# Kernel optimization log

Hardware: AMD Instinct MI355X
Metric: run time of the kernel (lower is better)

## Reference

```python
import jax, jax.numpy as jnp
import numpy as np

VOCAB, HID, L, HEADS, INTER, MAXSEQ, NCLS = 30522, 128, 2, 2, 512, 512, 2
HEAD = HID // HEADS
B, S = 128, 512


def _tlin(x, W, b):
    # TernaryLinear: threshold-quantize W to {-1,0,1} with per-tensor scale,
    # then ordinary linear. delta = 0.7*mean|W|, alpha = mean|W| over kept entries.
    absW = jnp.abs(W)
    delta = 0.7 * jnp.mean(absW)
    mask = (absW > delta).astype(W.dtype)
    alpha = jnp.sum(absW * mask) / jnp.maximum(jnp.sum(mask), 1.0)
    Wq = jnp.sign(W) * mask * alpha  # [out, in]
    return jnp.einsum('...i,oi->...o', x, Wq) + b


def _ln(x, g, b, eps=1e-5):
    m = jnp.mean(x, axis=-1, keepdims=True)
    v = jnp.var(x, axis=-1, keepdims=True)
    return (x - m) * jax.lax.rsqrt(v + eps) * g + b


def setup_inputs() -> dict:
    key = jax.random.key(0)
    ks = iter(jax.random.split(key, 64))
    n = lambda shape, s=0.02: jax.random.normal(next(ks), shape, dtype=jnp.float32) * s
    inp = {
        'input_ids': jax.random.randint(next(ks), (B, S), 0, VOCAB, dtype=jnp.int32).astype(jnp.int64),
        'tok_emb': n((VOCAB, HID)),
        'pos_emb': n((MAXSEQ, HID)),
        'ln_g': jnp.ones((HID,), jnp.float32), 'ln_b': jnp.zeros((HID,), jnp.float32),
        'qw': n((L, HID, HID)), 'qb': jnp.zeros((L, HID), jnp.float32),
        'kw': n((L, HID, HID)), 'kb': jnp.zeros((L, HID), jnp.float32),
        'vw': n((L, HID, HID)), 'vb': jnp.zeros((L, HID), jnp.float32),
        'aow': n((L, HID, HID)), 'aob': jnp.zeros((L, HID), jnp.float32),
        'iw': n((L, INTER, HID)), 'ib': jnp.zeros((L, INTER), jnp.float32),
        'fow': n((L, HID, INTER)), 'fob': jnp.zeros((L, HID), jnp.float32),
        'ln1g': jnp.ones((L, HID), jnp.float32), 'ln1b': jnp.zeros((L, HID), jnp.float32),
        'ln2g': jnp.ones((L, HID), jnp.float32), 'ln2b': jnp.zeros((L, HID), jnp.float32),
        'clf_w': n((NCLS, HID)), 'clf_b': jnp.zeros((NCLS,), jnp.float32),
    }
    return inp


def reference(input_ids, tok_emb, pos_emb, ln_g, ln_b, qw, qb, kw, kb, vw, vb,
              aow, aob, iw, ib, fow, fob, ln1g, ln1b, ln2g, ln2b, clf_w, clf_b):
    b, s = input_ids.shape
    x = tok_emb[input_ids] + pos_emb[jnp.arange(s)][None, :, :]  # [B,S,H]
    x = _ln(x, ln_g, ln_b)
    scale = 1.0 / (HEAD ** 0.5)
    for l in range(L):
        q = _tlin(x, qw[l], qb[l]).reshape(b, s, HEADS, HEAD)
        k = _tlin(x, kw[l], kb[l]).reshape(b, s, HEADS, HEAD)
        v = _tlin(x, vw[l], vb[l]).reshape(b, s, HEADS, HEAD)
        scores = jnp.einsum('bqhd,bkhd->bhqk', q, k) * scale
        attn = jax.nn.softmax(scores, axis=-1)
        ctx = jnp.einsum('bhqk,bkhd->bqhd', attn, v).reshape(b, s, HID)
        attn_out = _tlin(ctx, aow[l], aob[l])
        x = _ln(x + attn_out, ln1g[l], ln1b[l])
        ff = _tlin(jax.nn.relu(_tlin(x, iw[l], ib[l])), fow[l], fob[l])
        x = _ln(x + ff, ln2g[l], ln2b[l])
    cls = x[:, 0, :]
    logits = _tlin(cls, clf_w, clf_b)  # [B, NCLS]
    return logits
```

## Files before the change

kernel.cpp:

```cpp
#include <hip/hip_runtime.h>

typedef short bf8s __attribute__((ext_vector_type(8)));
typedef float f32x4 __attribute__((ext_vector_type(4)));

#define MFMA16(a, b, c) __builtin_amdgcn_mfma_f32_16x16x32_bf16(a, b, c, 0, 0, 0)

constexpr int S_ = 512, HID_ = 128, B_ = 128, M_ = B_ * S_;

__device__ inline short f2bf(float f) {
  unsigned u = __float_as_uint(f);
  u = (u + 0x7fffu + ((u >> 16) & 1u)) >> 16;
  return (short)u;
}
__device__ inline float bf2f(short s) {
  return __uint_as_float(((unsigned)(unsigned short)s) << 16);
}

__device__ __forceinline__ void async16(void* lds, const void* g) {
  __builtin_amdgcn_global_load_lds(
      (const __attribute__((address_space(1))) unsigned int*)g,
      (__attribute__((address_space(3))) unsigned int*)lds, 16, 0, 0);
}

__device__ __forceinline__ bf8s ldsb(const short* base, int byteoff) {
  return *(const bf8s*)((const char*)base + byteoff);
}

__device__ inline float block_red1024(float v, float* red) {
  #pragma unroll
  for (int m = 32; m >= 1; m >>= 1) v += __shfl_xor(v, m);
  __syncthreads();
  if ((threadIdx.x & 63) == 0) red[threadIdx.x >> 6] = v;
  __syncthreads();
  float t = 0.f;
  #pragma unroll
  for (int i = 0; i < 16; ++i) t += red[i];
  return t;
}

__device__ inline void mat_info(int mat, const float* qw, const float* kw,
                                const float* vw, const float* aow, const float* iw,
                                const float* fw, const float* cw,
                                const float** src, int* n, int* doff, int* lc) {
  if (mat < 6) {
    int l = mat / 3, which = mat % 3;
    const float* t[3] = {qw, kw, vw};
    *src = t[which] + l * 16384; *n = 16384; *doff = l * 49152 + which * 16384;
    *lc = 7;
  } else if (mat < 8) {
    int l = mat - 6;
    *src = aow + l * 16384; *n = 16384; *doff = 98304 + l * 16384; *lc = 7;
  } else if (mat < 10) {
    *src = iw + (mat - 8) * 65536; *n = 65536; *doff = 131072 + (mat - 8) * 65536;
    *lc = 7;
  } else if (mat < 12) {
    *src = fw + (mat - 10) * 65536; *n = 65536; *doff = 262144 + (mat - 10) * 65536;
    *lc = 9;
  } else {
    *src = cw; *n = 256; *doff = 393216; *lc = 0;
  }
}

__global__ __launch_bounds__(1024) void k_qe(const float* qw, const float* kw,
    const float* vw, const float* aow, const float* iw, const float* fw,
    const float* cw, short* WQ,
    const int* __restrict__ ids, const float* __restrict__ tok,
    const float* __restrict__ pos, const float* __restrict__ g,
    const float* __restrict__ bb, short* xb) {
  __shared__ float red[16];
  int tid = threadIdx.x;
  if (blockIdx.x < 13) {
    const float* src; int n, doff, lc;
    mat_info(blockIdx.x, qw, kw, vw, aow, iw, fw, cw, &src, &n, &doff, &lc);
    float s = 0.f;
    if (n >= 8192) {
      for (int i0 = tid; i0 < n; i0 += 8192) {
        float v[8];
        #pragma unroll
        for (int j = 0; j < 8; ++j) v[j] = src[i0 + j * 1024];
        #pragma unroll
        for (int j = 0; j < 8; ++j) s += fabsf(v[j]);
      }
    } else {
      for (int i = tid; i < n; i += 1024) s += fabsf(src[i]);
    }
    s = block_red1024(s, red);
    float delta = 0.7f * s / (float)n;
    float s2 = 0.f, c2 = 0.f;
    if (n >= 8192) {
      for (int i0 = tid; i0 < n; i0 += 8192) {
        float v[8];
        #pragma unroll
        for (int j = 0; j < 8; ++j) v[j] = src[i0 + j * 1024];
        #pragma unroll
        for (int j = 0; j < 8; ++j) {
          float a = fabsf(v[j]);
          s2 += (a > delta) ? a : 0.f;
          c2 += (a > delta) ? 1.f : 0.f;
        }
      }
    } else {
      for (int i = tid; i < n; i += 1024) {
        float a = fabsf(src[i]);
        if (a > delta) { s2 += a; c2 += 1.f; }
      }
    }
    s2 = block_red1024(s2, red);
    c2 = block_red1024(c2, red);
    float alpha = s2 / fmaxf(c2, 1.f);
    if (lc) {
      int nf8 = n >> 3;
      for (int fo8 = tid; fo8 < nf8; fo8 += 1024) {
        int fo = fo8 << 3;
        int tile = fo >> (lc + 4);
        int rem = fo & ((16 << lc) - 1);
        int kblk = rem >> 9;
        int rem2 = rem & 511;
        int sub = rem2 >> 7;
        int r16 = (rem2 >> 3) & 15;
        int r = (tile << 4) | r16;
        int cbase = (kblk << 5) | (sub << 3);
        const float* sp = src + ((size_t)r << lc) + cbase;
        float4 w0 = *(const float4*)(sp);
        float4 w1 = *(const float4*)(sp + 4);
        float wv[8] = {w0.x, w0.y, w0.z, w0.w, w1.x, w1.y, w1.z, w1.w};
        bf8s q;
        #pragma unroll
        for (int j = 0; j < 8; ++j) {
          float w = wv[j];
          q[j] = (fabsf(w) > delta) ? f2bf(w > 0.f ? alpha : -alpha) : (short)0;
        }
        *(bf8s*)(WQ + doff + fo) = q;
      }
    } else {
      for (int i = tid; i < n; i += 1024) {
        float w = src[i];
        WQ[doff + i] = (fabsf(w) > delta) ? f2bf(w > 0.f ? alpha : -alpha) : (short)0;
      }
    }
  } else {
    int wave = tid >> 6, lane = tid & 63;
    int half = lane >> 5, l32 = lane & 31;
    int t = (blockIdx.x - 13) * 32 + wave * 2 + half;
    int s = t & (S_ - 1);
    int id = ids[t];
    int d0 = l32 * 4;
    float4 te = *(const float4*)(tok + (size_t)id * HID_ + d0);
    float4 pe = *(const float4*)(pos + (size_t)s * HID_ + d0);
    float e0 = te.x + pe.x, e1 = te.y + pe.y, e2 = te.z + pe.z, e3 = te.w + pe.w;
    float sum = e0 + e1 + e2 + e3;
    float ssq = e0 * e0 + e1 * e1 + e2 * e2 + e3 * e3;
    #pragma unroll
    for (int m = 16; m >= 1; m >>= 1) {
      sum += __shfl_xor(sum, m);
      ssq += __shfl_xor(ssq, m);
    }
    float mean = sum / 128.f;
    float var = ssq / 128.f - mean * mean;
    float rs = rsqrtf(var + 1e-5f);
    float4 g4 = *(const float4*)(g + d0);
    float4 b4 = *(const float4*)(bb + d0);
    short4 o;
    o.x = f2bf((e0 - mean) * rs * g4.x + b4.x);
    o.y = f2bf((e1 - mean) * rs * g4.y + b4.y);
    o.z = f2bf((e2 - mean) * rs * g4.z + b4.z);
    o.w = f2bf((e3 - mean) * rs * g4.w + b4.w);
    *(short4*)(xb + (size_t)t * HID_ + d0) = o;
  }
}

__global__ __launch_bounds__(256) void k_qkv(
    const short* __restrict__ A, const short* __restrict__ W,
    const float* __restrict__ b0, const float* __restrict__ b1,
    const float* __restrict__ b2, short* outb) {
  __shared__ short Wl[16384];
  int tid = threadIdx.x, lane = tid & 63, wave = tid >> 6;
  int row16 = lane & 15, quad = lane >> 4;
  int tok0 = blockIdx.x * 64 + wave * 16;

  const char* Wm = (const char*)W + blockIdx.y * 32768;
  #pragma unroll
  for (int t = 0; t < 8; ++t)
    async16((char*)Wl + t * 4096 + wave * 1024,
            Wm + t * 4096 + wave * 1024 + lane * 16);

  const short* arow = A + (size_t)(tok0 + row16) * 128 + quad * 8;
  bf8s av[4];
  #pragma unroll
  for (int ki = 0; ki < 4; ++ki) av[ki] = *(const bf8s*)(arow + ki * 32);
  __syncthreads();

  f32x4 acc[8] = {};
  #pragma unroll
  for (int ki = 0; ki < 4; ++ki)
    #pragma unroll
    for (int ot = 0; ot < 8; ++ot) {
      bf8s b = ldsb(Wl, ot * 4096 + ki * 1024 + lane * 16);
      acc[ot] = MFMA16(av[ki], b, acc[ot]);
    }
  __syncthreads();

  const float* bp = (blockIdx.y == 0) ? b0 : ((blockIdx.y == 1) ? b1 : b2);
  float osc = (blockIdx.y == 0) ? 0.125f : 1.0f;
  short* scr = Wl + wave * 2112;
  #pragma unroll
  for (int ot = 0; ot < 8; ++ot) {
    int col = ot * 16 + row16;
    float bi = bp[col];
    #pragma unroll
    for (int r = 0; r < 4; ++r)
      scr[(quad * 4 + r) * 132 + col] = f2bf((acc[ot][r] + bi) * osc);
  }
  {
    int rr = lane >> 2, cg = lane & 3;
    const short* src = scr + rr * 132 + cg * 32;
    short* dst = outb + (size_t)(tok0 + rr) * 384 + blockIdx.y * 128 + cg * 32;
    #pragma unroll
    for (int j = 0; j < 4; ++j)
      *(bf8s*)(dst + j * 8) = *(const bf8s*)(src + j * 8);
  }
}

template <int DOQKV>
__global__ __launch_bounds__(512, 4) void k_aoff(
    const short* __restrict__ cb, const short* __restrict__ Wa,
    const float* __restrict__ aob, const float* __restrict__ ln1g,
    const float* __restrict__ ln1b, const short* __restrict__ Wi,
    const short* __restrict__ Wf, const float* __restrict__ ib,
    const float* __restrict__ fb, const float* __restrict__ ln2g,
    const float* __restrict__ ln2b, short* xb,
    const short* __restrict__ Wqkv2, const float* __restrict__ qb2,
    const float* __restrict__ kb2, const float* __restrict__ vb2,
    short* qkvout) {
  __shared__ short SM[39936];
  int tid = threadIdx.x, lane = tid & 63, wave = tid >> 6;
  int row16 = lane & 15, quad = lane >> 4;
  int tok0 = blockIdx.x * 128 + wave * 16;
  short* mySt = SM + 16384 + wave * 640;
  short* myX  = SM + 21504 + wave * 2304;
  int xr = lane >> 2, xs = (lane & 3) * 32;
  int lb = lane * 16;

  {
    #pragma unroll
    for (int t = 0; t < 4; ++t)
      async16((char*)SM + t * 8192 + wave * 1024,
              (const char*)Wa + t * 8192 + wave * 1024 + lb);
    const short* src = xb + (size_t)(tok0 + xr) * HID_ + xs;
    bf8s x0 = *(const bf8s*)(src);
    bf8s x1 = *(const bf8s*)(src + 8);
    bf8s x2 = *(const bf8s*)(src + 16);
    bf8s x3 = *(const bf8s*)(src + 24);
    short* dst = myX + xr * 144 + xs;
    *(bf8s*)(dst) = x0;      *(bf8s*)(dst + 8) = x1;
    *(bf8s*)(dst + 16) = x2; *(bf8s*)(dst + 24) = x3;
  }

  const short* arow = cb + (size_t)(tok0 + row16) * 128 + quad * 8;
  bf8s av[4];
  #pragma unroll
  for (int ki = 0; ki < 4; ++ki) av[ki] = *(const bf8s*)(arow + ki * 32);
  __syncthreads();

  f32x4 acc[8] = {};
  #pragma unroll
  for (int ki = 0; ki < 4; ++ki)
    #pragma unroll
    for (int ot = 0; ot < 8; ++ot) {
      bf8s b = ldsb(SM, ot * 4096 + ki * 1024 + lb);
      acc[ot] = MFMA16(av[ki], b, acc[ot]);
    }
  __syncthreads();

  {
    async16((char*)SM + wave * 1024, (const char*)Wi + wave * 1024 + lb);
    async16((char*)SM + 16384 + wave * 1024,
            (const char*)Wf + wave * 16384 + lb);
  }

  {
    float sum[4] = {}, ssq[4] = {};
    #pragma unroll
    for (int ot = 0; ot < 8; ++ot) {
      int col = ot * 16 + row16;
      float bi = aob[col];
      #pragma unroll
      for (int r = 0; r < 4; ++r) {
        float v = acc[ot][r] + bi + bf2f(myX[(quad * 4 + r) * 144 + col]);
        acc[ot][r] = v;
        sum[r] += v; ssq[r] += v * v;
      }
    }
    #pragma unroll
    for (int m = 1; m <= 8; m <<= 1)
      #pragma unroll
      for (int r = 0; r < 4; ++r) {
        sum[r] += __shfl_xor(sum[r], m);
        ssq[r] += __shfl_xor(ssq[r], m);
      }
    float mean[4], rstd[4];
    #pragma unroll
    for (int r = 0; r < 4; ++r) {
      mean[r] = sum[r] / 128.f;
      float var = ssq[r] / 128.f - mean[r] * mean[r];
      rstd[r] = rsqrtf(var + 1e-5f);
    }
    #pragma unroll
    for (int ot = 0; ot < 8; ++ot) {
      int col = ot * 16 + row16;
      float gg = ln1g[col], bb2 = ln1b[col];
      #pragma unroll
      for (int r = 0; r < 4; ++r)
        acc[ot][r] = (acc[ot][r] - mean[r]) * rstd[r] * gg + bb2;
    }
  }

  #pragma unroll
  for (int ot = 0; ot < 8; ++ot) {
    int col = ot * 16 + row16;
    #pragma unroll
    for (int r = 0; r < 4; ++r)
      myX[(quad * 4 + r) * 144 + col] = f2bf(acc[ot][r]);
  }
  #pragma unroll
  for (int ki = 0; ki < 4; ++ki)
    av[ki] = *(const bf8s*)(myX + row16 * 144 + ki * 32 + quad * 8);
  __syncthreads();

  f32x4 acc2[8] = {};
  for (int c = 0; c < 16; ++c) {
    int side = c & 1;
    if (c < 15) {
      int cn = c + 1, sn = cn & 1;
      async16((char*)SM + sn * 8192 + wave * 1024,
              (const char*)Wi + cn * 8192 + wave * 1024 + lb);
      async16((char*)SM + 16384 + sn * 8192 + wave * 1024,
              (const char*)Wf + wave * 16384 + cn * 1024 + lb);
    } else if (DOQKV) {
      async16((char*)SM + wave * 1024, (const char*)Wqkv2 + wave * 1024 + lb);
      async16((char*)SM + 16384 + wave * 1024,
              (const char*)Wqkv2 + 8192 + wave * 1024 + lb);
    }

    #pragma unroll
    for (int ot = 0; ot < 2; ++ot) {
      f32x4 hacc = {};
      #pragma unroll
      for (int ki = 0; ki < 4; ++ki) {
        bf8s b = ldsb(SM, side * 8192 + ot * 4096 + ki * 1024 + lb);
        hacc = MFMA16(av[ki], b, hacc);
      }
      float bi = ib[c * 32 + ot * 16 + row16];
      #pragma unroll
      for (int r = 0; r < 4; ++r)
        mySt[(quad * 4 + r) * 40 + ot * 16 + row16] =
            f2bf(fmaxf(hacc[r] + bi, 0.f));
    }
    bf8s ha = *(const bf8s*)(mySt + row16 * 40 + quad * 8);
    #pragma unroll
    for (int ot = 0; ot < 8; ++ot) {
      bf8s bB = ldsb(SM, 16384 + side * 8192 + ot * 1024 + lb);
      acc2[ot] = MFMA16(ha, bB, acc2[ot]);
    }
    __syncthreads();
  }

  {
    float sum[4] = {}, ssq[4] = {};
    #pragma unroll
    for (int ot = 0; ot < 8; ++ot) {
      int col = ot * 16 + row16;
      float bi = fb[col];
      #pragma unroll
      for (int r = 0; r < 4; ++r) {
        float v = acc2[ot][r] + bi + bf2f(myX[(quad * 4 + r) * 144 + col]);
        acc2[ot][r] = v;
        sum[r] += v; ssq[r] += v * v;
      }
    }
    #pragma unroll
    for (int m = 1; m <= 8; m <<= 1)
      #pragma unroll
      for (int r = 0; r < 4; ++r) {
        sum[r] += __shfl_xor(sum[r], m);
        ssq[r] += __shfl_xor(ssq[r], m);
      }
    float mean[4], rstd[4];
    #pragma unroll
    for (int r = 0; r < 4; ++r) {
      mean[r] = sum[r] / 128.f;
      float var = ssq[r] / 128.f - mean[r] * mean[r];
      rstd[r] = rsqrtf(var + 1e-5f);
    }
    #pragma unroll
    for (int ot = 0; ot < 8; ++ot) {
      int col = ot * 16 + row16;
      float gg = ln2g[col], bb2 = ln2b[col];
      #pragma unroll
      for (int r = 0; r < 4; ++r)
        acc2[ot][r] = (acc2[ot][r] - mean[r]) * rstd[r] * gg + bb2;
    }
  }

  #pragma unroll
  for (int ot = 0; ot < 8; ++ot) {
    int col = ot * 16 + row16;
    #pragma unroll
    for (int r = 0; r < 4; ++r)
      myX[(quad * 4 + r) * 144 + col] = f2bf(acc2[ot][r]);
  }
  {
    const short* src = myX + xr * 144 + xs;
    short* dst = xb + (size_t)(tok0 + xr) * HID_ + xs;
    #pragma unroll
    for (int j = 0; j < 4; ++j)
      *(bf8s*)(dst + j * 8) = *(const bf8s*)(src + j * 8);
  }

  if (DOQKV) {
    bf8s av2[4];
    #pragma unroll
    for (int ki = 0; ki < 4; ++ki)
      av2[ki] = *(const bf8s*)(myX + row16 * 144 + ki * 32 + quad * 8);
    for (int j = 0; j < 6; ++j) {
      int side = j & 1;
      if (j < 5) {
        int jn = j + 1, sn = jn & 1;
        async16((char*)SM + sn * 8192 + wave * 1024,
                (const char*)Wqkv2 + jn * 16384 + wave * 1024 + lb);
        async16((char*)SM + 16384 + sn * 8192 + wave * 1024,
                (const char*)Wqkv2 + jn * 16384 + 8192 + wave * 1024 + lb);
      }
      f32x4 acc3[4] = {};
      #pragma unroll
      for (int ki = 0; ki < 4; ++ki)
        #pragma unroll
        for (int ot = 0; ot < 4; ++ot) {
          int bb_ = (ot < 2) ? side * 8192 + ot * 4096
                             : 16384 + side * 8192 + (ot - 2) * 4096;
          bf8s b = ldsb(SM, bb_ + ki * 1024 + lb);
          acc3[ot] = MFMA16(av2[ki], b, acc3[ot]);
        }
      const float* bp = (j < 2) ? qb2 : ((j < 4) ? kb2 : vb2);
      float osc = (j < 2) ? 0.125f : 1.0f;
      #pragma unroll
      for (int ot = 0; ot < 4; ++ot) {
        int col = ot * 16 + row16;
        float bi = bp[(j & 1) * 64 + col];
        #pragma unroll
        for (int r = 0; r < 4; ++r)
          myX[(quad * 4 + r) * 144 + col] = f2bf((acc3[ot][r] + bi) * osc);
      }
      {
        int xr2 = lane >> 2, xs2 = (lane & 3) * 16;
        const short* src = myX + xr2 * 144 + xs2;
        short* dst = qkvout + (size_t)(tok0 + xr2) * 384 + j * 64 + xs2;
        *(bf8s*)(dst) = *(const bf8s*)(src);
        *(bf8s*)(dst + 8) = *(const bf8s*)(src + 8);
      }
      __syncthreads();
    }
  }
}

__global__ __launch_bounds__(512) void k_attn(const short* __restrict__ qkv,
                                              short* __restrict__ O) {
  __shared__ short Kl[64 * 72];
  __shared__ short Vtl[64 * 72];
  __shared__ short Pl[8][16 * 72];

  int tid = threadIdx.x, lane = tid & 63, wave = tid >> 6;
  int row16 = lane & 15, quad = lane >> 4;
  int b = blockIdx.x >> 2, h = (blockIdx.x >> 1) & 1, qhalf = blockIdx.x & 1;
  const short* base  = qkv + (size_t)b * S_ * 384;
  const short* kbase = base + 128 + h * 64;
  const short* vbase = base + 256 + h * 64;
  int q0 = qhalf * 256 + wave * 32;

  bf8s qa[2][2];
  #pragma unroll
  for (int qf = 0; qf < 2; ++qf) {
    const short* qrow = base + h * 64 +
        (size_t)(q0 + qf * 16 + row16) * 384 + quad * 8;
    qa[qf][0] = *(const bf8s*)(qrow);
    qa[qf][1] = *(const bf8s*)(qrow + 32);
  }

  int krow = tid >> 3, dgk = tid & 7;
  int vkey = tid & 63, dgv = tid >> 6;
  const short* kptr = kbase + (size_t)krow * 384 + dgk * 8;
  const short* vptr = vbase + (size_t)vkey * 384 + dgv * 8;
  bf8s kst = *(const bf8s*)(kptr);
  bf8s vst = *(const bf8s*)(vptr);

  float li[2][4] = {};
  f32x4 oacc[2][4] = {};
  short* myP = &Pl[wave][0];

  for (int kt0 = 0; kt0 < S_; kt0 += 64) {
    if (kt0) __syncthreads();
    *(bf8s*)(&Kl[krow * 72 + dgk * 8]) = kst;
    #pragma unroll
    for (int j = 0; j < 8; ++j) Vtl[(dgv * 8 + j) * 72 + vkey] = vst[j];
    __syncthreads();
    if (kt0 + 64 < S_) {
      kst = *(const bf8s*)(kptr + (size_t)(kt0 + 64) * 384);
      vst = *(const bf8s*)(vptr + (size_t)(kt0 + 64) * 384);
    }

    f32x4 sc[2][4] = {};
    #pragma unroll
    for (int ks = 0; ks < 4; ++ks) {
      const short* kp = &Kl[(ks * 16 + row16) * 72 + quad * 8];
      bf8s k0 = *(const bf8s*)(kp);
      bf8s k1 = *(const bf8s*)(kp + 32);
      sc[0][ks] = MFMA16(qa[0][0], k0, sc[0][ks]);
      sc[0][ks] = MFMA16(qa[0][1], k1, sc[0][ks]);
      sc[1][ks] = MFMA16(qa[1][0], k0, sc[1][ks]);
      sc[1][ks] = MFMA16(qa[1][1], k1, sc[1][ks]);
    }

    #pragma unroll
    for (int qf = 0; qf < 2; ++qf) {
      #pragma unroll
      for (int ks = 0; ks < 4; ++ks)
        #pragma unroll
        for (int r = 0; r < 4; ++r) {
          float pv = __expf(sc[qf][ks][r]);
          li[qf][r] += pv;
          myP[(quad * 4 + r) * 72 + ks * 16 + row16] = f2bf(pv);
        }
      bf8s pa0 = *(const bf8s*)(&myP[row16 * 72 + quad * 8]);
      bf8s pa1 = *(const bf8s*)(&myP[row16 * 72 + 32 + quad * 8]);
      #pragma unroll
      for (int dt = 0; dt < 4; ++dt) {
        const short* vp = &Vtl[(dt * 16 + row16) * 72 + quad * 8];
        bf8s v0 = *(const bf8s*)(vp);
        bf8s v1 = *(const bf8s*)(vp + 32);
        oacc[qf][dt] = MFMA16(pa0, v0, oacc[qf][dt]);
        oacc[qf][dt] = MFMA16(pa1, v1, oacc[qf][dt]);
      }
    }
  }

  #pragma unroll
  for (int qf = 0; qf < 2; ++qf) {
    float inv[4];
    #pragma unroll
    for (int r = 0; r < 4; ++r) {
      float t = li[qf][r];
      #pragma unroll
      for (int m = 1; m <= 8; m <<= 1) t += __shfl_xor(t, m);
      inv[r] = 1.f / t;
    }
    size_t trow = (size_t)(b * S_ + q0 + qf * 16 + quad * 4);
    #pragma unroll
    for (int dt = 0; dt < 4; ++dt)
      #pragma unroll
      for (int r = 0; r < 4; ++r)
        O[(trow + r) * HID_ + h * 64 + dt * 16 + row16] =
            f2bf(oacc[qf][dt][r] * inv[r]);
  }
}

__global__ __launch_bounds__(64) void k_clf(const short* __restrict__ xb,
    const short* __restrict__ Wc, const float* __restrict__ cbias, float* out) {
  int b = blockIdx.x, lane = threadIdx.x;
  const short* xr = xb + (size_t)b * S_ * HID_;
  float x0 = bf2f(xr[lane * 2]), x1 = bf2f(xr[lane * 2 + 1]);
  #pragma unroll
  for (int c = 0; c < 2; ++c) {
    float s = x0 * bf2f(Wc[c * HID_ + lane * 2]) +
              x1 * bf2f(Wc[c * HID_ + lane * 2 + 1]);
    #pragma unroll
    for (int m = 32; m >= 1; m >>= 1) s += __shfl_xor(s, m);
    if (lane == 0) out[b * 2 + c] = s + cbias[c];
  }
}

extern "C" void kernel_launch(void* const* d_in, const int* in_sizes, int n_in,
                              void* d_out, int out_size, void* d_ws, size_t ws_size,
                              hipStream_t stream) {
  const int*   ids     = (const int*)d_in[0];
  const float* tok_emb = (const float*)d_in[1];
  const float* pos_emb = (const float*)d_in[2];
  const float* ln_g    = (const float*)d_in[3];
  const float* ln_bb   = (const float*)d_in[4];
  const float* qw      = (const float*)d_in[5];
  const float* qbias   = (const float*)d_in[6];
  const float* kw      = (const float*)d_in[7];
  const float* kbias   = (const float*)d_in[8];
  const float* vw      = (const float*)d_in[9];
  const float* vbias   = (const float*)d_in[10];
  const float* aow     = (const float*)d_in[11];
  const float* aobias  = (const float*)d_in[12];
  const float* iw      = (const float*)d_in[13];
  const float* ibias   = (const float*)d_in[14];
  const float* fow     = (const float*)d_in[15];
  const float* fbias   = (const float*)d_in[16];
  const float* ln1g    = (const float*)d_in[17];
  const float* ln1b    = (const float*)d_in[18];
  const float* ln2g    = (const float*)d_in[19];
  const float* ln2b    = (const float*)d_in[20];
  const float* clfw    = (const float*)d_in[21];
  const float* clfb    = (const float*)d_in[22];

  char* ws = (char*)d_ws;
  short* WQ  = (short*)ws;
  short* xb  = (short*)(ws + 1048576);
  short* qkv = (short*)(ws + 1048576 + 16777216);
  short* cb_ = qkv + (size_t)M_ * 384;

  k_qe<<<13 + M_ / 32, 1024, 0, stream>>>(qw, kw, vw, aow, iw, fow, clfw, WQ,
                                          ids, tok_emb, pos_emb, ln_g, ln_bb, xb);

  const short* Wqkv0 = WQ;
  const short* Wqkv1 = WQ + 49152;
  const short* Wa0   = WQ + 98304;
  const short* Wa1   = WQ + 98304 + 16384;
  const short* Wi0   = WQ + 131072;
  const short* Wi1   = WQ + 131072 + 65536;
  const short* Wf0   = WQ + 262144;
  const short* Wf1   = WQ + 262144 + 65536;

  k_qkv<<<dim3(M_ / 64, 3), 256, 0, stream>>>(
      xb, Wqkv0, qbias, kbias, vbias, qkv);
  k_attn<<<512, 512, 0, stream>>>(qkv, cb_);
  k_aoff<1><<<M_ / 128, 512, 0, stream>>>(
      cb_, Wa0, aobias, ln1g, ln1b, Wi0, Wf0, ibias, fbias, ln2g, ln2b, xb,
      Wqkv1, qbias + HID_, kbias + HID_, vbias + HID_, qkv);
  k_attn<<<512, 512, 0, stream>>>(qkv, cb_);
  k_aoff<0><<<M_ / 128, 512, 0, stream>>>(
      cb_, Wa1, aobias + HID_, ln1g + HID_, ln1b + HID_, Wi1, Wf1,
      ibias + 512, fbias + HID_, ln2g + HID_, ln2b + HID_, xb,
      nullptr, nullptr, nullptr, nullptr, nullptr);

  k_clf<<<128, 64, 0, stream>>>(xb, WQ + 393216, clfb, (float*)d_out);
}
```

Baseline: 295.5 us.

## Fuse Q/K/V projections into one block with double-buffered weight chunks

The layer-0 QKV projection kernel drops its 3-wide grid dimension. Each block now loads its 64-token activation tile into registers once and loops over six 64-column weight chunks, prefetching the next chunk into a second LDS buffer with async global-to-LDS loads while the current one feeds the MFMAs. This cuts activation reads from global memory to a third and overlaps weight staging with compute. The cost is a third as many blocks, so less parallelism, plus a barrier on every chunk iteration.

```diff
diff --git a/kernel.cpp b/kernel.cpp
--- a/kernel.cpp
+++ b/kernel.cpp
@@ -6,6 +6,7 @@
 #define MFMA16(a, b, c) __builtin_amdgcn_mfma_f32_16x16x32_bf16(a, b, c, 0, 0, 0)
 
 constexpr int S_ = 512, HID_ = 128, B_ = 128, M_ = B_ * S_;
+
 
 __device__ inline short f2bf(float f) {
   unsigned u = __float_as_uint(f);
@@ -173,16 +174,17 @@
     const short* __restrict__ A, const short* __restrict__ W,
     const float* __restrict__ b0, const float* __restrict__ b1,
     const float* __restrict__ b2, short* outb) {
-  __shared__ short Wl[16384];
+  __shared__ short SM[25088];
   int tid = threadIdx.x, lane = tid & 63, wave = tid >> 6;
   int row16 = lane & 15, quad = lane >> 4;
   int tok0 = blockIdx.x * 64 + wave * 16;
-
-  const char* Wm = (const char*)W + blockIdx.y * 32768;
-  #pragma unroll
-  for (int t = 0; t < 8; ++t)
-    async16((char*)Wl + t * 4096 + wave * 1024,
-            Wm + t * 4096 + wave * 1024 + lane * 16);
+  short* scr = SM + 16384 + wave * 2176;
+  int lb = lane * 16;
+
+  #pragma unroll
+  for (int t = 0; t < 4; ++t)
+    async16((char*)SM + (wave * 4 + t) * 1024,
+            (const char*)W + (wave * 4 + t) * 1024 + lb);
 
   const short* arow = A + (size_t)(tok0 + row16) * 128 + quad * 8;
   bf8s av[4];
@@ -190,34 +192,43 @@
   for (int ki = 0; ki < 4; ++ki) av[ki] = *(const bf8s*)(arow + ki * 32);
   __syncthreads();
 
-  f32x4 acc[8] = {};
-  #pragma unroll
-  for (int ki = 0; ki < 4; ++ki)
-    #pragma unroll
-    for (int ot = 0; ot < 8; ++ot) {
-      bf8s b = ldsb(Wl, ot * 4096 + ki * 1024 + lane * 16);
-      acc[ot] = MFMA16(av[ki], b, acc[ot]);
-    }
-  __syncthreads();
-
-  const float* bp = (blockIdx.y == 0) ? b0 : ((blockIdx.y == 1) ? b1 : b2);
-  float osc = (blockIdx.y == 0) ? 0.125f : 1.0f;
-  short* scr = Wl + wave * 2112;
-  #pragma unroll
-  for (int ot = 0; ot < 8; ++ot) {
-    int col = ot * 16 + row16;
-    float bi = bp[col];
-    #pragma unroll
-    for (int r = 0; r < 4; ++r)
-      scr[(quad * 4 + r) * 132 + col] = f2bf((acc[ot][r] + bi) * osc);
-  }
-  {
-    int rr = lane >> 2, cg = lane & 3;
-    const short* src = scr + rr * 132 + cg * 32;
-    short* dst = outb + (size_t)(tok0 + rr) * 384 + blockIdx.y * 128 + cg * 32;
-    #pragma unroll
-    for (int j = 0; j < 4; ++j)
-      *(bf8s*)(dst + j * 8) = *(const bf8s*)(src + j * 8);
+  for (int j = 0; j < 6; ++j) {
+    int side = j & 1;
+    if (j < 5) {
+      int jn = j + 1, sn = jn & 1;
+      #pragma unroll
+      for (int t = 0; t < 4; ++t)
+        async16((char*)SM + sn * 16384 + (wave * 4 + t) * 1024,
+                (const char*)W + jn * 16384 + (wave * 4 + t) * 1024 + lb);
+    }
+    f32x4 acc[4] = {};
+    #pragma unroll
+    for (int ki = 0; ki < 4; ++ki)
+      #pragma unroll
+      for (int ot = 0; ot < 4; ++ot) {
+        bf8s b = ldsb(SM, side * 16384 + ot * 4096 + ki * 1024 + lb);
+        acc[ot] = MFMA16(av[ki], b, acc[ot]);
+      }
+    int mtx = j >> 1;
+    const float* bp = (mtx == 0) ? b0 : ((mtx == 1) ? b1 : b2);
+    float osc = (mtx == 0) ? 0.125f : 1.0f;
+    #pragma unroll
+    for (int ot = 0; ot < 4; ++ot) {
+      int col = ot * 16 + row16;
+      float bi = bp[(j & 1) * 64 + col];
+      #pragma unroll
+      for (int r = 0; r < 4; ++r)
+        scr[(quad * 4 + r) * 136 + col] = f2bf((acc[ot][r] + bi) * osc);
+    }
+    {
+      int xr2 = lane >> 2, xs2 = (lane & 3) * 16;
+      const short* src = scr + xr2 * 136 + xs2;
+      short* dst = outb + (size_t)(tok0 + xr2) * 384 + mtx * 128 +
+                   (j & 1) * 64 + xs2;
+      *(bf8s*)(dst) = *(const bf8s*)(src);
+      *(bf8s*)(dst + 8) = *(const bf8s*)(src + 8);
+    }
+    __syncthreads();
   }
 }
 
@@ -623,7 +634,7 @@
   const short* Wf0   = WQ + 262144;
   const short* Wf1   = WQ + 262144 + 65536;
 
-  k_qkv<<<dim3(M_ / 64, 3), 256, 0, stream>>>(
+  k_qkv<<<M_ / 64, 256, 0, stream>>>(
       xb, Wqkv0, qbias, kbias, vbias, qkv);
   k_attn<<<512, 512, 0, stream>>>(qkv, cb_);
   k_aoff<1><<<M_ / 128, 512, 0, stream>>>(
```

Result: no change. 297.6 us, median of 2 (+0.7%).
